# Performance work log

Measured on AMD Instinct MI355X. Metric: run time of the kernel, lower is better.

The kernel has to match this reference:

```python
import jax, jax.numpy as jnp
import numpy as np

EPS = 1e-8  # matches torch F.cosine_similarity eps


def setup_inputs() -> dict:
    key = jax.random.key(0)
    k1, = jax.random.split(key, 1)
    N, U, D = 512, 32, 512
    embeddings = jax.random.normal(k1, (N, U, D), dtype=jnp.float32)
    w = jnp.asarray(10.0, dtype=jnp.float32)  # init_w
    b = jnp.asarray(-5.0, dtype=jnp.float32)  # init_b
    return {"embeddings": embeddings, "w": w, "b": b}


def reference(embeddings, w, b):
    N, U, D = embeddings.shape
    # centroids per speaker (mean over utterances; module includes current utt)
    centroids = embeddings.mean(axis=1)  # (N, D)
    # cosine similarity via normalize + matmul
    e = embeddings.reshape(N * U, D)
    e_n = e / jnp.maximum(jnp.linalg.norm(e, axis=-1, keepdims=True), EPS)
    c_n = centroids / jnp.maximum(
        jnp.linalg.norm(centroids, axis=-1, keepdims=True), EPS)
    sim = (e_n @ c_n.T).reshape(N, U, N)  # (N, U, N)
    sim = w * sim + b
    logp = jax.nn.log_softmax(sim, axis=-1)  # (N, U, N)
    # pick logp[j, k, j] for every j, k
    diag = jnp.take_along_axis(
        logp, jnp.arange(N)[:, None, None], axis=2)[..., 0]  # (N, U)
    return -diag.mean()
```

## Files before the change

kernel.cpp:

```cpp
#include <hip/hip_runtime.h>
#include <math.h>

#define N_SPK 512
#define N_UTT 32
#define DIM   512
#define EPSN  1e-8f

typedef __attribute__((ext_vector_type(8))) short  short8;
typedef __attribute__((ext_vector_type(4))) float  f32x4;

__device__ inline unsigned short f2bf(float x) {
  unsigned int u = __builtin_bit_cast(unsigned int, x);
  unsigned int r = (u + 0x7fffu + ((u >> 16) & 1u)) >> 16;
  return (unsigned short)r;
}

__global__ __launch_bounds__(256) void centroid_kernel(
    const float* __restrict__ emb, unsigned short* __restrict__ cn) {
  int j = blockIdx.x;
  int t = threadIdx.x;
  const float* base = emb + (size_t)j * N_UTT * DIM;
  float s0 = 0.f, s1 = 0.f;
#pragma unroll
  for (int u = 0; u < N_UTT; ++u) {
    s0 += base[u * DIM + t];
    s1 += base[u * DIM + t + 256];
  }
  s0 *= (1.f / N_UTT);
  s1 *= (1.f / N_UTT);
  float ss = s0 * s0 + s1 * s1;
#pragma unroll
  for (int off = 32; off > 0; off >>= 1) ss += __shfl_xor(ss, off, 64);
  __shared__ float red[4];
  if ((t & 63) == 0) red[t >> 6] = ss;
  __syncthreads();
  float total = red[0] + red[1] + red[2] + red[3];
  float inv = 1.f / fmaxf(sqrtf(total), EPSN);
  cn[(size_t)j * DIM + t]       = f2bf(s0 * inv);
  cn[(size_t)j * DIM + t + 256] = f2bf(s1 * inv);
}

__global__ __launch_bounds__(256, 3) void ge2e_kernel(
    const float* __restrict__ emb, const unsigned short* __restrict__ cn,
    const float* __restrict__ wp, const float* __restrict__ bp,
    float* __restrict__ out) {
  __shared__ __align__(16) unsigned short E[N_UTT * DIM];
  __shared__ float red[4][N_UTT][2];
  __shared__ float dred[4];

  int j = blockIdx.x;
  int t = threadIdx.x;
  int lane = t & 63, wid = t >> 6;
  int n15 = lane & 15, quad = lane >> 4;

#pragma unroll
  for (int r8 = 0; r8 < 8; ++r8) {
    int r = wid * 8 + r8;
    const float* rp = emb + ((size_t)j * N_UTT + r) * DIM + lane * 8;
    float4 v0 = *(const float4*)rp;
    float4 v1 = *(const float4*)(rp + 4);
    float ss = v0.x * v0.x + v0.y * v0.y + v0.z * v0.z + v0.w * v0.w +
               v1.x * v1.x + v1.y * v1.y + v1.z * v1.z + v1.w * v1.w;
#pragma unroll
    for (int off = 32; off > 0; off >>= 1) ss += __shfl_xor(ss, off, 64);
    float inv = 1.f / fmaxf(sqrtf(ss), EPSN);
    short8 pk;
    pk[0] = (short)f2bf(v0.x * inv); pk[1] = (short)f2bf(v0.y * inv);
    pk[2] = (short)f2bf(v0.z * inv); pk[3] = (short)f2bf(v0.w * inv);
    pk[4] = (short)f2bf(v1.x * inv); pk[5] = (short)f2bf(v1.y * inv);
    pk[6] = (short)f2bf(v1.z * inv); pk[7] = (short)f2bf(v1.w * inv);
    int sw = lane ^ (r & 7);
    *(short8*)&E[r * DIM + sw * 8] = pk;
  }
  __syncthreads();

  f32x4 acc[2][8];
#pragma unroll
  for (int mt = 0; mt < 2; ++mt)
#pragma unroll
    for (int nt = 0; nt < 8; ++nt) acc[mt][nt] = (f32x4){0.f, 0.f, 0.f, 0.f};

  for (int ks = 0; ks < 16; ++ks) {
    short8 b[8];
#pragma unroll
    for (int nt = 0; nt < 8; ++nt) {
      int c = wid * 128 + nt * 16 + n15;
      b[nt] = *(const short8*)(cn + (size_t)c * DIM + ks * 32 + quad * 8);
    }
    short8 a[2];
#pragma unroll
    for (int mt = 0; mt < 2; ++mt) {
      int r = mt * 16 + n15;
      int sw = (ks * 4 + quad) ^ (r & 7);
      a[mt] = *(const short8*)&E[r * DIM + sw * 8];
    }
#pragma unroll
    for (int mt = 0; mt < 2; ++mt)
#pragma unroll
      for (int nt = 0; nt < 8; ++nt)
        acc[mt][nt] = __builtin_amdgcn_mfma_f32_16x16x32_bf16(
            a[mt], b[nt], acc[mt][nt], 0, 0, 0);
  }

  float w = *wp, bb = *bp;
  float dsum = 0.f;
#pragma unroll
  for (int mt = 0; mt < 2; ++mt)
#pragma unroll
    for (int nt = 0; nt < 8; ++nt) {
      int c = wid * 128 + nt * 16 + n15;
      bool isdiag = (c == j);
#pragma unroll
      for (int rg = 0; rg < 4; ++rg) {
        float v = fmaf(w, acc[mt][nt][rg], bb);
        acc[mt][nt][rg] = v;
        if (isdiag) dsum += v;
      }
    }

#pragma unroll
  for (int mt = 0; mt < 2; ++mt)
#pragma unroll
    for (int rg = 0; rg < 4; ++rg) {
      float m = -INFINITY;
#pragma unroll
      for (int nt = 0; nt < 8; ++nt) m = fmaxf(m, acc[mt][nt][rg]);
#pragma unroll
      for (int off = 1; off < 16; off <<= 1) m = fmaxf(m, __shfl_xor(m, off, 64));
      float s = 0.f;
#pragma unroll
      for (int nt = 0; nt < 8; ++nt) s += __expf(acc[mt][nt][rg] - m);
#pragma unroll
      for (int off = 1; off < 16; off <<= 1) s += __shfl_xor(s, off, 64);
      if (n15 == 0) {
        int r = mt * 16 + quad * 4 + rg;
        red[wid][r][0] = m;
        red[wid][r][1] = s;
      }
    }
#pragma unroll
  for (int off = 32; off > 0; off >>= 1) dsum += __shfl_xor(dsum, off, 64);
  if (lane == 0) dred[wid] = dsum;
  __syncthreads();

  if (t < 32) {
    float M = -INFINITY;
#pragma unroll
    for (int ww = 0; ww < 4; ++ww) M = fmaxf(M, red[ww][t][0]);
    float S = 0.f;
#pragma unroll
    for (int ww = 0; ww < 4; ++ww) S += red[ww][t][1] * __expf(red[ww][t][0] - M);
    float lse = M + __logf(S);
#pragma unroll
    for (int off = 16; off > 0; off >>= 1) lse += __shfl_xor(lse, off, 64);
    if (t == 0) {
      float tot = lse - (dred[0] + dred[1] + dred[2] + dred[3]);
      atomicAdd(out, tot * (1.f / (N_SPK * N_UTT)));
    }
  }
}

extern "C" void kernel_launch(void* const* d_in, const int* in_sizes, int n_in,
                              void* d_out, int out_size, void* d_ws, size_t ws_size,
                              hipStream_t stream) {
  const float* emb = (const float*)d_in[0];
  const float* wp  = (const float*)d_in[1];
  const float* bp  = (const float*)d_in[2];
  float* out = (float*)d_out;
  unsigned short* cn = (unsigned short*)d_ws;

  hipMemsetAsync(d_out, 0, sizeof(float), stream);
  centroid_kernel<<<N_SPK, 256, 0, stream>>>(emb, cn);
  ge2e_kernel<<<N_SPK, 256, 0, stream>>>(emb, cn, wp, bp, out);
}
```

Measured before the change: 114.6 us.

## Use k-chunked centroid layout, 512-thread GE2E blocks, deterministic finalize reduction

The centroid kernel now reads with float4 loads and writes the normalized centroids in a k-chunk-major layout ([16][512][32]), so each MFMA B-fragment load reads contiguous 64-byte runs instead of strided rows. The main kernel moves from 4 to 8 waves per block, each wave covering 64 centroid columns, to raise occupancy and latency hiding. The memset plus atomicAdd is replaced by per-block partials and a small finalize kernel. This adds one extra kernel launch and more cross-wave shared-memory reduction in exchange for better memory coalescing and more parallelism.

```diff
diff --git a/kernel.cpp b/kernel.cpp
--- a/kernel.cpp
+++ b/kernel.cpp
@@ -15,20 +15,32 @@
   return (unsigned short)r;
 }
 
+#define CNK_ELEMS (N_SPK * DIM)
+
 __global__ __launch_bounds__(256) void centroid_kernel(
-    const float* __restrict__ emb, unsigned short* __restrict__ cn) {
-  int j = blockIdx.x;
-  int t = threadIdx.x;
-  const float* base = emb + (size_t)j * N_UTT * DIM;
-  float s0 = 0.f, s1 = 0.f;
-#pragma unroll
-  for (int u = 0; u < N_UTT; ++u) {
-    s0 += base[u * DIM + t];
-    s1 += base[u * DIM + t + 256];
-  }
-  s0 *= (1.f / N_UTT);
-  s1 *= (1.f / N_UTT);
-  float ss = s0 * s0 + s1 * s1;
+    const float* __restrict__ emb, unsigned short* __restrict__ cnk) {
+  int j = blockIdx.x, t = threadIdx.x;
+  int c4 = t & 127, half = t >> 7;
+  const float4* base = (const float4*)(emb + (size_t)j * N_UTT * DIM);
+  float4 s = {0.f, 0.f, 0.f, 0.f};
+#pragma unroll
+  for (int u = 0; u < 16; ++u) {
+    float4 v = base[(half + 2 * u) * 128 + c4];
+    s.x += v.x; s.y += v.y; s.z += v.z; s.w += v.w;
+  }
+  __shared__ float4 comb[128];
+  if (half) comb[c4] = s;
+  __syncthreads();
+  float4 m = {0.f, 0.f, 0.f, 0.f};
+  float ss = 0.f;
+  if (!half) {
+    float4 o = comb[c4];
+    m.x = (s.x + o.x) * (1.f / N_UTT);
+    m.y = (s.y + o.y) * (1.f / N_UTT);
+    m.z = (s.z + o.z) * (1.f / N_UTT);
+    m.w = (s.w + o.w) * (1.f / N_UTT);
+    ss = m.x * m.x + m.y * m.y + m.z * m.z + m.w * m.w;
+  }
 #pragma unroll
   for (int off = 32; off > 0; off >>= 1) ss += __shfl_xor(ss, off, 64);
   __shared__ float red[4];
@@ -36,17 +48,22 @@
   __syncthreads();
   float total = red[0] + red[1] + red[2] + red[3];
   float inv = 1.f / fmaxf(sqrtf(total), EPSN);
-  cn[(size_t)j * DIM + t]       = f2bf(s0 * inv);
-  cn[(size_t)j * DIM + t + 256] = f2bf(s1 * inv);
-}
-
-__global__ __launch_bounds__(256, 3) void ge2e_kernel(
-    const float* __restrict__ emb, const unsigned short* __restrict__ cn,
+  if (!half) {
+    int d0 = c4 * 4;
+    int kc = d0 >> 5;
+    unsigned short* p = cnk + ((size_t)kc * N_SPK + j) * 32 + (d0 & 31);
+    p[0] = f2bf(m.x * inv); p[1] = f2bf(m.y * inv);
+    p[2] = f2bf(m.z * inv); p[3] = f2bf(m.w * inv);
+  }
+}
+
+__global__ __launch_bounds__(512, 4) void ge2e_kernel(
+    const float* __restrict__ emb, const unsigned short* __restrict__ cnk,
     const float* __restrict__ wp, const float* __restrict__ bp,
-    float* __restrict__ out) {
+    float* __restrict__ partials) {
   __shared__ __align__(16) unsigned short E[N_UTT * DIM];
-  __shared__ float red[4][N_UTT][2];
-  __shared__ float dred[4];
+  __shared__ float red[8][N_UTT][2];
+  __shared__ float dred[8];
 
   int j = blockIdx.x;
   int t = threadIdx.x;
@@ -54,8 +71,8 @@
   int n15 = lane & 15, quad = lane >> 4;
 
 #pragma unroll
-  for (int r8 = 0; r8 < 8; ++r8) {
-    int r = wid * 8 + r8;
+  for (int r8 = 0; r8 < 4; ++r8) {
+    int r = wid * 4 + r8;
     const float* rp = emb + ((size_t)j * N_UTT + r) * DIM + lane * 8;
     float4 v0 = *(const float4*)rp;
     float4 v1 = *(const float4*)(rp + 4);
@@ -74,18 +91,18 @@
   }
   __syncthreads();
 
-  f32x4 acc[2][8];
+  f32x4 acc[2][4];
 #pragma unroll
   for (int mt = 0; mt < 2; ++mt)
 #pragma unroll
-    for (int nt = 0; nt < 8; ++nt) acc[mt][nt] = (f32x4){0.f, 0.f, 0.f, 0.f};
+    for (int nt = 0; nt < 4; ++nt) acc[mt][nt] = (f32x4){0.f, 0.f, 0.f, 0.f};
 
   for (int ks = 0; ks < 16; ++ks) {
-    short8 b[8];
-#pragma unroll
-    for (int nt = 0; nt < 8; ++nt) {
-      int c = wid * 128 + nt * 16 + n15;
-      b[nt] = *(const short8*)(cn + (size_t)c * DIM + ks * 32 + quad * 8);
+    short8 b[4];
+#pragma unroll
+    for (int nt = 0; nt < 4; ++nt) {
+      int c = wid * 64 + nt * 16 + n15;
+      b[nt] = *(const short8*)(cnk + ((size_t)ks * N_SPK + c) * 32 + quad * 8);
     }
     short8 a[2];
 #pragma unroll
@@ -97,7 +114,7 @@
 #pragma unroll
     for (int mt = 0; mt < 2; ++mt)
 #pragma unroll
-      for (int nt = 0; nt < 8; ++nt)
+      for (int nt = 0; nt < 4; ++nt)
         acc[mt][nt] = __builtin_amdgcn_mfma_f32_16x16x32_bf16(
             a[mt], b[nt], acc[mt][nt], 0, 0, 0);
   }
@@ -107,8 +124,8 @@
 #pragma unroll
   for (int mt = 0; mt < 2; ++mt)
 #pragma unroll
-    for (int nt = 0; nt < 8; ++nt) {
-      int c = wid * 128 + nt * 16 + n15;
+    for (int nt = 0; nt < 4; ++nt) {
+      int c = wid * 64 + nt * 16 + n15;
       bool isdiag = (c == j);
 #pragma unroll
       for (int rg = 0; rg < 4; ++rg) {
@@ -124,12 +141,12 @@
     for (int rg = 0; rg < 4; ++rg) {
       float m = -INFINITY;
 #pragma unroll
-      for (int nt = 0; nt < 8; ++nt) m = fmaxf(m, acc[mt][nt][rg]);
+      for (int nt = 0; nt < 4; ++nt) m = fmaxf(m, acc[mt][nt][rg]);
 #pragma unroll
       for (int off = 1; off < 16; off <<= 1) m = fmaxf(m, __shfl_xor(m, off, 64));
       float s = 0.f;
 #pragma unroll
-      for (int nt = 0; nt < 8; ++nt) s += __expf(acc[mt][nt][rg] - m);
+      for (int nt = 0; nt < 4; ++nt) s += __expf(acc[mt][nt][rg] - m);
 #pragma unroll
       for (int off = 1; off < 16; off <<= 1) s += __shfl_xor(s, off, 64);
       if (n15 == 0) {
@@ -146,17 +163,33 @@
   if (t < 32) {
     float M = -INFINITY;
 #pragma unroll
-    for (int ww = 0; ww < 4; ++ww) M = fmaxf(M, red[ww][t][0]);
+    for (int ww = 0; ww < 8; ++ww) M = fmaxf(M, red[ww][t][0]);
     float S = 0.f;
 #pragma unroll
-    for (int ww = 0; ww < 4; ++ww) S += red[ww][t][1] * __expf(red[ww][t][0] - M);
+    for (int ww = 0; ww < 8; ++ww) S += red[ww][t][1] * __expf(red[ww][t][0] - M);
     float lse = M + __logf(S);
 #pragma unroll
     for (int off = 16; off > 0; off >>= 1) lse += __shfl_xor(lse, off, 64);
     if (t == 0) {
-      float tot = lse - (dred[0] + dred[1] + dred[2] + dred[3]);
-      atomicAdd(out, tot * (1.f / (N_SPK * N_UTT)));
-    }
+      float d = dred[0] + dred[1] + dred[2] + dred[3] +
+                dred[4] + dred[5] + dred[6] + dred[7];
+      partials[j] = lse - d;
+    }
+  }
+}
+
+__global__ __launch_bounds__(512) void finalize_kernel(
+    const float* __restrict__ partials, float* __restrict__ out) {
+  int t = threadIdx.x;
+  float v = partials[t];
+#pragma unroll
+  for (int off = 32; off > 0; off >>= 1) v += __shfl_xor(v, off, 64);
+  __shared__ float r[8];
+  if ((t & 63) == 0) r[t >> 6] = v;
+  __syncthreads();
+  if (t == 0) {
+    float s = r[0] + r[1] + r[2] + r[3] + r[4] + r[5] + r[6] + r[7];
+    out[0] = s * (1.f / (N_SPK * N_UTT));
   }
 }
 
@@ -167,9 +200,10 @@
   const float* wp  = (const float*)d_in[1];
   const float* bp  = (const float*)d_in[2];
   float* out = (float*)d_out;
-  unsigned short* cn = (unsigned short*)d_ws;
-
-  hipMemsetAsync(d_out, 0, sizeof(float), stream);
-  centroid_kernel<<<N_SPK, 256, 0, stream>>>(emb, cn);
-  ge2e_kernel<<<N_SPK, 256, 0, stream>>>(emb, cn, wp, bp, out);
-}
+  unsigned short* cnk = (unsigned short*)d_ws;
+  float* partials = (float*)((char*)d_ws + (size_t)CNK_ELEMS * 2);
+
+  centroid_kernel<<<N_SPK, 256, 0, stream>>>(emb, cnk);
+  ge2e_kernel<<<N_SPK, 512, 0, stream>>>(emb, cnk, wp, bp, partials);
+  finalize_kernel<<<1, 512, 0, stream>>>(partials, out);
+}
```

Measured after the change: 97.33 us. 1.18x faster.
